# Optimization experiments

Hardware: AMD Instinct MI355X
Metric: run time of the kernel (lower is better)

Reference implementation:

```python
import jax, jax.numpy as jnp
import numpy as np

HEAD_SIZE = 64   # baseChn * max_channel_ratio
NUM_HEADS = 2
LEAKY_ALPHA = 0.3  # tf.keras.layers.LeakyReLU default


def setup_inputs() -> dict:
    key = jax.random.key(0)
    ks = jax.random.split(key, 6)
    x = jax.random.normal(ks[0], (96, 48, 512), dtype=jnp.float32)
    y = jax.random.uniform(ks[1], (96, 64, 64), dtype=jnp.float32)
    nItem = jax.random.uniform(ks[2], (96,), dtype=jnp.float32, minval=1.0, maxval=48.0)
    W_proj = jax.random.normal(ks[3], (512, 64), dtype=jnp.float32) * 0.05
    W1 = jax.random.normal(ks[4], (64, 128), dtype=jnp.float32) * 0.1
    W2 = jax.random.normal(ks[5], (2, 1), dtype=jnp.float32)
    return {"x": x, "y": y, "nItem": nItem, "W_proj": W_proj, "W1": W1, "W2": W2}


def reference(x, y, nItem, W_proj, W1, W2):
    # fc_cnn_proj: Dense(64, gelu exact, no bias)
    gallery = jax.nn.gelu(jnp.matmul(x, W_proj), approximate=False)  # [Sx, Nx, 64]
    Sx, Nx, _ = gallery.shape
    Sy, Ny, _ = y.shape
    sqrt_hs = jnp.sqrt(jnp.float32(HEAD_SIZE))
    # shared linear (no bias) then split heads: [S, H, N, hs]
    px = jnp.matmul(gallery, W1).reshape(Sx, Nx, NUM_HEADS, HEAD_SIZE).transpose(0, 2, 1, 3)
    py = jnp.matmul(y, W1).reshape(Sy, Ny, NUM_HEADS, HEAD_SIZE).transpose(0, 2, 1, 3)
    # pairwise cross-set attention maps: [Sy, Sx, H, Ny, Nx]
    att = jnp.einsum('yhmd,xhnd->yxhmn', py, px) / sqrt_hs
    att = jnp.where(att > 0, att, LEAKY_ALPHA * att)
    # reduce over both item axes, normalize by nItem[x] and nItemMax_y
    sc = att.sum(axis=(3, 4)) / nItem[None, :, None] / jnp.float32(Ny)  # [Sy, Sx, H]
    scores = jnp.matmul(sc, W2)  # linear2: Dense(1, no bias) -> [Sy, Sx, 1]
    return scores
```

## Files before the change

kernel.cpp:

```cpp
#include <hip/hip_runtime.h>
#include <hip/hip_bf16.h>


typedef short bf16x8 __attribute__((ext_vector_type(8)));
typedef float f32x4 __attribute__((ext_vector_type(4)));

__device__ __forceinline__ unsigned short f2bf(float v) {
  __hip_bfloat16 b = __float2bfloat16(v);
  return *reinterpret_cast<unsigned short*>(&b);
}

__device__ __forceinline__ bf16x8 load8_cvt(const float* __restrict__ p) {
  f32x4 v0 = *reinterpret_cast<const f32x4*>(p);
  f32x4 v1 = *reinterpret_cast<const f32x4*>(p + 4);
  bf16x8 r;
  r[0] = (short)f2bf(v0[0]); r[1] = (short)f2bf(v0[1]);
  r[2] = (short)f2bf(v0[2]); r[3] = (short)f2bf(v0[3]);
  r[4] = (short)f2bf(v1[0]); r[5] = (short)f2bf(v1[1]);
  r[6] = (short)f2bf(v1[2]); r[7] = (short)f2bf(v1[3]);
  return r;
}

__global__ __launch_bounds__(256) void k_wprep(const float* __restrict__ Wp,
                                               const float* __restrict__ W1,
                                               unsigned short* __restrict__ WpF,
                                               unsigned short* __restrict__ W1F) {
  int tid = blockIdx.x * 256 + threadIdx.x;
  if (tid < 32768) {
    int kc = tid >> 11, nt = (tid >> 9) & 3, l = (tid >> 3) & 63, i = tid & 7;
    int k = 32 * kc + 8 * (l >> 4) + i, c = nt * 16 + (l & 15);
    WpF[tid] = f2bf(Wp[k * 64 + c]);
  } else {
    int t2 = tid - 32768;
    int kc = t2 >> 12, nt = (t2 >> 9) & 7, l = (t2 >> 3) & 63, i = t2 & 7;
    int k = 32 * kc + 8 * (l >> 4) + i, d = nt * 16 + (l & 15);
    W1F[t2] = f2bf(W1[k * 128 + d]);
  }
}

__global__ __launch_bounds__(256, 3) void k_prep2(const float* __restrict__ x,
                                                  const float* __restrict__ y,
                                                  const unsigned short* __restrict__ WpF_u,
                                                  const unsigned short* __restrict__ W1F_u,
                                                  unsigned short* __restrict__ pyf,
                                                  unsigned short* __restrict__ pxf) {
  __shared__ unsigned short w1f[8192];
  __shared__ unsigned short wpq[16384];
  __shared__ unsigned short gal[32 * 72];
  int t = threadIdx.x;
  int lane = t & 63, w = t >> 6;
  int b = blockIdx.x;

  const bf16x8* W1Fg = reinterpret_cast<const bf16x8*>(W1F_u);
  const bf16x8* WPFg = reinterpret_cast<const bf16x8*>(WpF_u);
  const bf16x8* WF = reinterpret_cast<const bf16x8*>(w1f);
  const bf16x8* WPQ = reinterpret_cast<const bf16x8*>(wpq);

#pragma unroll
  for (int it = 0; it < 4; ++it)
    reinterpret_cast<bf16x8*>(w1f)[it * 256 + t] = W1Fg[it * 256 + t];

  f32x4 zero4 = {0.f, 0.f, 0.f, 0.f};
  asm volatile("" : "+v"(zero4));

  if (b < 144) {
    int rowbase = b * 32;
    int rt = w & 1, ntp = (w >> 1) * 2;
    const float* xa = x + (size_t)(rowbase + rt * 16 + (lane & 15)) * 512 + 8 * (lane >> 4);
    f32x4 acc[2] = {{0, 0, 0, 0}, {0, 0, 0, 0}};
#pragma unroll
    for (int hf = 0; hf < 2; ++hf) {
      if (hf) __syncthreads();
#pragma unroll
      for (int it = 0; it < 8; ++it)
        reinterpret_cast<bf16x8*>(wpq)[it * 256 + t] = WPFg[hf * 2048 + it * 256 + t];
      __syncthreads();
#pragma unroll
      for (int kcl = 0; kcl < 8; ++kcl) {
        bf16x8 a = load8_cvt(xa + 32 * (hf * 8 + kcl));
#pragma unroll
        for (int u = 0; u < 2; ++u)
          acc[u] = __builtin_amdgcn_mfma_f32_16x16x32_bf16(a, WPQ[(kcl * 4 + ntp + u) * 64 + lane], acc[u], 0, 0, 0);
      }
    }
#pragma unroll
    for (int u = 0; u < 2; ++u)
#pragma unroll
      for (int j = 0; j < 4; ++j) {
        float s = acc[u][j];
        float ge = 0.5f * s * (1.0f + erff(s * 0.70710678118654752f));
        int lr = rt * 16 + (lane >> 4) * 4 + j;
        int c = (ntp + u) * 16 + (lane & 15);
        gal[lr * 72 + c] = f2bf(ge);
      }
    __syncthreads();
    int nb = (w >> 1) * 4;
    const unsigned short* gp = &gal[(rt * 16 + (lane & 15)) * 72 + 8 * (lane >> 4)];
    bf16x8 g0 = *reinterpret_cast<const bf16x8*>(gp);
    bf16x8 g1 = *reinterpret_cast<const bf16x8*>(gp + 32);
#pragma unroll
    for (int v = 0; v < 4; ++v) {
      int nt2 = nb + v;
      f32x4 acc2 = __builtin_amdgcn_mfma_f32_16x16x32_bf16(g0, WF[nt2 * 64 + lane], zero4, 0, 0, 0);
      acc2 = __builtin_amdgcn_mfma_f32_16x16x32_bf16(g1, WF[(8 + nt2) * 64 + lane], acc2, 0, 0, 0);
      int d = nt2 * 16 + (lane & 15);
      int h = d >> 6, dd = d & 63;
      int kc = dd >> 5, q2 = (dd >> 3) & 3, i = dd & 7;
#pragma unroll
      for (int j = 0; j < 4; ++j) {
        int row = rowbase + rt * 16 + (lane >> 4) * 4 + j;
        int xi = row / 48, n = row % 48;
        int nt3 = n >> 4, rr = n & 15;
        size_t idx = ((size_t)((xi * 2 + h) * 6 + nt3 * 2 + kc)) * 512 + (rr + (q2 << 4)) * 8 + i;
        pxf[idx] = f2bf(acc2[j]);
      }
    }
  } else {
    __syncthreads();
    int b2 = b - 144;
    int mt = w & 1, nb = (w >> 1) * 4;
    const float* ybp = y + (size_t)(b2 * 32 + mt * 16 + (lane & 15)) * 64 + 8 * (lane >> 4);
    bf16x8 a0 = load8_cvt(ybp);
    bf16x8 a1 = load8_cvt(ybp + 32);
#pragma unroll
    for (int v = 0; v < 4; ++v) {
      int nt2 = nb + v;
      f32x4 acc = __builtin_amdgcn_mfma_f32_16x16x32_bf16(a0, WF[nt2 * 64 + lane], zero4, 0, 0, 0);
      acc = __builtin_amdgcn_mfma_f32_16x16x32_bf16(a1, WF[(8 + nt2) * 64 + lane], acc, 0, 0, 0);
      int d = nt2 * 16 + (lane & 15);
      int h = d >> 6, dd = d & 63;
      int kc = dd >> 5, q2 = (dd >> 3) & 3, i = dd & 7;
#pragma unroll
      for (int j = 0; j < 4; ++j) {
        int row = b2 * 32 + mt * 16 + (lane >> 4) * 4 + j;
        int yi = row >> 6, m = row & 63;
        int mt3 = m >> 4, rr = m & 15;
        size_t idx = ((size_t)((yi * 2 + h) * 8 + mt3 * 2 + kc)) * 512 + (rr + (q2 << 4)) * 8 + i;
        pyf[idx] = f2bf(acc[j]);
      }
    }
  }
}

__global__ __launch_bounds__(256) void k_att(const unsigned short* __restrict__ pyf_u,
                                             const unsigned short* __restrict__ pxf_u,
                                             const float* __restrict__ nItem,
                                             const float* __restrict__ W2,
                                             float* __restrict__ out) {
  int lane = threadIdx.x & 63;
  int w = threadIdx.x >> 6;
  int bid = blockIdx.x;
  int yb = bid >> 5, xq = bid & 31;
  int yi = yb * 4 + w;
  int xi0 = xq * 3;
  const bf16x8* PA = reinterpret_cast<const bf16x8*>(pyf_u);
  const bf16x8* PB = reinterpret_cast<const bf16x8*>(pxf_u);

  float w2h0 = W2[0], w2h1 = W2[1];
  float nI0 = nItem[xi0], nI1 = nItem[xi0 + 1], nI2 = nItem[xi0 + 2];

  f32x4 zero4 = {0.f, 0.f, 0.f, 0.f};
  asm volatile("" : "+v"(zero4));

  bf16x8 A8[16];
  size_t abase = (size_t)(yi * 2) * 512 + lane;
#pragma unroll
  for (int f = 0; f < 8; ++f) {
    A8[f]     = PA[abase + f * 64];
    A8[8 + f] = PA[abase + 512 + f * 64];
  }
  float c3h0 = 0.3f * w2h0, c7h0 = 0.7f * w2h0;
  float c3h1 = 0.3f * w2h1, c7h1 = 0.7f * w2h1;

  bf16x8 Bc[6], Bn[6];
  size_t bb0 = (size_t)((xi0 * 2 + 0) * 6) * 64 + lane;
#pragma unroll
  for (int f = 0; f < 6; ++f) Bc[f] = PB[bb0 + f * 64];

  f32x4 res4[3];
#pragma unroll
  for (int g = 0; g < 3; ++g) res4[g] = (f32x4){0.f, 0.f, 0.f, 0.f};

#pragma unroll
  for (int s = 0; s < 6; ++s) {
    const int h = s / 3, g = s % 3;
    if (s < 5) {
      const int s2 = s + 1, h2 = s2 / 3, g2 = s2 % 3;
      size_t bb = (size_t)(((xi0 + g2) * 2 + h2) * 6) * 64 + lane;
#pragma unroll
      for (int f = 0; f < 6; ++f) Bn[f] = PB[bb + f * 64];
    }
    const float c3 = h ? c3h1 : c3h0;
    const float c7 = h ? c7h1 : c7h0;
#pragma unroll
    for (int nt = 0; nt < 3; ++nt)
#pragma unroll
      for (int mt = 0; mt < 4; ++mt) {
        f32x4 acc = __builtin_amdgcn_mfma_f32_16x16x32_bf16(A8[h * 8 + mt * 2], Bc[nt * 2], zero4, 0, 0, 0);
        acc = __builtin_amdgcn_mfma_f32_16x16x32_bf16(A8[h * 8 + mt * 2 + 1], Bc[nt * 2 + 1], acc, 0, 0, 0);
        f32x4 mx = {fmaxf(acc[0], 0.f), fmaxf(acc[1], 0.f), fmaxf(acc[2], 0.f), fmaxf(acc[3], 0.f)};
        res4[g] += acc * c3;
        res4[g] += mx * c7;
      }
#pragma unroll
    for (int f = 0; f < 6; ++f) Bc[f] = Bn[f];
  }

  float tot0 = (res4[0][0] + res4[0][1]) + (res4[0][2] + res4[0][3]);
  float tot1 = (res4[1][0] + res4[1][1]) + (res4[1][2] + res4[1][3]);
  float tot2 = (res4[2][0] + res4[2][1]) + (res4[2][2] + res4[2][3]);
#pragma unroll
  for (int off = 32; off >= 1; off >>= 1) {
    tot0 += __shfl_xor(tot0, off, 64);
    tot1 += __shfl_xor(tot1, off, 64);
    tot2 += __shfl_xor(tot2, off, 64);
  }
  if (lane == 0) {
    out[yi * 96 + xi0 + 0] = tot0 / (512.0f * nI0);
    out[yi * 96 + xi0 + 1] = tot1 / (512.0f * nI1);
    out[yi * 96 + xi0 + 2] = tot2 / (512.0f * nI2);
  }
}

extern "C" void kernel_launch(void* const* d_in, const int* in_sizes, int n_in,
                              void* d_out, int out_size, void* d_ws, size_t ws_size,
                              hipStream_t stream) {
  const float* x     = (const float*)d_in[0];
  const float* y     = (const float*)d_in[1];
  const float* nItem = (const float*)d_in[2];
  const float* Wp    = (const float*)d_in[3];
  const float* W1    = (const float*)d_in[4];
  const float* W2    = (const float*)d_in[5];
  float* out = (float*)d_out;

  unsigned short* WpF = (unsigned short*)d_ws;
  unsigned short* W1F = WpF + 32768;
  unsigned short* pyf = W1F + 8192;
  unsigned short* pxf = pyf + 786432;

  hipLaunchKernelGGL(k_wprep, dim3(160), dim3(256), 0, stream, Wp, W1, WpF, W1F);
  hipLaunchKernelGGL(k_prep2, dim3(336), dim3(256), 0, stream, x, y, WpF, W1F, pyf, pxf);
  hipLaunchKernelGGL(k_att, dim3(768), dim3(256), 0, stream, pyf, pxf, nItem, W2, out);
}
```

Measured before the change: 38.64 us.

## Fuse weight bf16 conversion into prep kernel and drop separate weight-prep launch

Removes the standalone kernel that converted and reordered W_proj and W1 into bf16 MFMA fragment layout. Each prep block now reads the fp32 weights directly and converts and scatters them into shared memory itself, with W_proj staged in four quarter-sized chunks. This eliminates one kernel launch and its dependency barrier. In exchange, every one of the 336 blocks redoes the weight conversion, issuing scalar ushort scatter stores to LDS plus extra syncs.

```diff
diff --git a/kernel.cpp b/kernel.cpp
--- a/kernel.cpp
+++ b/kernel.cpp
@@ -21,44 +21,30 @@
   return r;
 }
 
-__global__ __launch_bounds__(256) void k_wprep(const float* __restrict__ Wp,
-                                               const float* __restrict__ W1,
-                                               unsigned short* __restrict__ WpF,
-                                               unsigned short* __restrict__ W1F) {
-  int tid = blockIdx.x * 256 + threadIdx.x;
-  if (tid < 32768) {
-    int kc = tid >> 11, nt = (tid >> 9) & 3, l = (tid >> 3) & 63, i = tid & 7;
-    int k = 32 * kc + 8 * (l >> 4) + i, c = nt * 16 + (l & 15);
-    WpF[tid] = f2bf(Wp[k * 64 + c]);
-  } else {
-    int t2 = tid - 32768;
-    int kc = t2 >> 12, nt = (t2 >> 9) & 7, l = (t2 >> 3) & 63, i = t2 & 7;
-    int k = 32 * kc + 8 * (l >> 4) + i, d = nt * 16 + (l & 15);
-    W1F[t2] = f2bf(W1[k * 128 + d]);
-  }
-}
-
-__global__ __launch_bounds__(256, 3) void k_prep2(const float* __restrict__ x,
+__global__ __launch_bounds__(256, 3) void k_prep3(const float* __restrict__ x,
                                                   const float* __restrict__ y,
-                                                  const unsigned short* __restrict__ WpF_u,
-                                                  const unsigned short* __restrict__ W1F_u,
+                                                  const float* __restrict__ Wp,
+                                                  const float* __restrict__ W1,
                                                   unsigned short* __restrict__ pyf,
                                                   unsigned short* __restrict__ pxf) {
   __shared__ unsigned short w1f[8192];
-  __shared__ unsigned short wpq[16384];
+  __shared__ unsigned short wpq[8192];
   __shared__ unsigned short gal[32 * 72];
   int t = threadIdx.x;
   int lane = t & 63, w = t >> 6;
   int b = blockIdx.x;
 
-  const bf16x8* W1Fg = reinterpret_cast<const bf16x8*>(W1F_u);
-  const bf16x8* WPFg = reinterpret_cast<const bf16x8*>(WpF_u);
   const bf16x8* WF = reinterpret_cast<const bf16x8*>(w1f);
   const bf16x8* WPQ = reinterpret_cast<const bf16x8*>(wpq);
 
 #pragma unroll
-  for (int it = 0; it < 4; ++it)
-    reinterpret_cast<bf16x8*>(w1f)[it * 256 + t] = W1Fg[it * 256 + t];
+  for (int it = 0; it < 32; ++it) {
+    int idx = it * 256 + t;
+    int k = idx >> 7, d = idx & 127;
+    int l = (d & 15) + 16 * ((k >> 3) & 3);
+    int f = (k >> 5) * 8 + (d >> 4);
+    w1f[f * 512 + l * 8 + (k & 7)] = f2bf(W1[idx]);
+  }
 
   f32x4 zero4 = {0.f, 0.f, 0.f, 0.f};
   asm volatile("" : "+v"(zero4));
@@ -69,18 +55,23 @@
     const float* xa = x + (size_t)(rowbase + rt * 16 + (lane & 15)) * 512 + 8 * (lane >> 4);
     f32x4 acc[2] = {{0, 0, 0, 0}, {0, 0, 0, 0}};
 #pragma unroll
-    for (int hf = 0; hf < 2; ++hf) {
-      if (hf) __syncthreads();
-#pragma unroll
-      for (int it = 0; it < 8; ++it)
-        reinterpret_cast<bf16x8*>(wpq)[it * 256 + t] = WPFg[hf * 2048 + it * 256 + t];
+    for (int q = 0; q < 4; ++q) {
+      if (q) __syncthreads();
+#pragma unroll
+      for (int it = 0; it < 32; ++it) {
+        int idx = it * 256 + t;
+        int kq = idx >> 6, c = idx & 63;
+        int l = (c & 15) + 16 * ((kq >> 3) & 3);
+        int g = ((kq >> 5) & 3) * 4 + (c >> 4);
+        wpq[g * 512 + l * 8 + (kq & 7)] = f2bf(Wp[(q * 128 + kq) * 64 + c]);
+      }
       __syncthreads();
 #pragma unroll
-      for (int kcl = 0; kcl < 8; ++kcl) {
-        bf16x8 a = load8_cvt(xa + 32 * (hf * 8 + kcl));
+      for (int kk = 0; kk < 4; ++kk) {
+        bf16x8 a = load8_cvt(xa + 32 * (q * 4 + kk));
 #pragma unroll
         for (int u = 0; u < 2; ++u)
-          acc[u] = __builtin_amdgcn_mfma_f32_16x16x32_bf16(a, WPQ[(kcl * 4 + ntp + u) * 64 + lane], acc[u], 0, 0, 0);
+          acc[u] = __builtin_amdgcn_mfma_f32_16x16x32_bf16(a, WPQ[(kk * 4 + ntp + u) * 64 + lane], acc[u], 0, 0, 0);
       }
     }
 #pragma unroll
@@ -233,12 +224,9 @@
   const float* W2    = (const float*)d_in[5];
   float* out = (float*)d_out;
 
-  unsigned short* WpF = (unsigned short*)d_ws;
-  unsigned short* W1F = WpF + 32768;
-  unsigned short* pyf = W1F + 8192;
+  unsigned short* pyf = (unsigned short*)d_ws;
   unsigned short* pxf = pyf + 786432;
 
-  hipLaunchKernelGGL(k_wprep, dim3(160), dim3(256), 0, stream, Wp, W1, WpF, W1F);
-  hipLaunchKernelGGL(k_prep2, dim3(336), dim3(256), 0, stream, x, y, WpF, W1F, pyf, pxf);
+  hipLaunchKernelGGL(k_prep3, dim3(336), dim3(256), 0, stream, x, y, Wp, W1, pyf, pxf);
   hipLaunchKernelGGL(k_att, dim3(768), dim3(256), 0, stream, pyf, pxf, nItem, W2, out);
 }
```

Result: slower. 48.47 us (+25.4%).

## Make projection kernel wave-independent, reading weights directly from global memory

Applied to the files above, without the earlier changes.

The projection kernel changes from block-cooperative tiles with weights staged in shared memory and block barriers to one 16-row tile per wavefront. Each wave computes all 64 gallery columns and all 128 projected columns itself, loading the weight fragments straight from global memory (L2/L1 cached), and uses a per-wave shared scratch for the GELU output with no __syncthreads. This removes the shared-memory weight staging and the block-level synchronisation, and shrinks LDS use so more blocks can be resident per CU. In exchange it issues more redundant global weight reads per wave, and each wave carries more accumulator registers and does more serial MFMA work.

```diff
diff --git a/kernel.cpp b/kernel.cpp
--- a/kernel.cpp
+++ b/kernel.cpp
@@ -38,77 +38,55 @@
   }
 }
 
-__global__ __launch_bounds__(256, 3) void k_prep2(const float* __restrict__ x,
-                                                  const float* __restrict__ y,
-                                                  const unsigned short* __restrict__ WpF_u,
-                                                  const unsigned short* __restrict__ W1F_u,
-                                                  unsigned short* __restrict__ pyf,
-                                                  unsigned short* __restrict__ pxf) {
-  __shared__ unsigned short w1f[8192];
-  __shared__ unsigned short wpq[16384];
-  __shared__ unsigned short gal[32 * 72];
-  int t = threadIdx.x;
-  int lane = t & 63, w = t >> 6;
-  int b = blockIdx.x;
-
-  const bf16x8* W1Fg = reinterpret_cast<const bf16x8*>(W1F_u);
-  const bf16x8* WPFg = reinterpret_cast<const bf16x8*>(WpF_u);
-  const bf16x8* WF = reinterpret_cast<const bf16x8*>(w1f);
-  const bf16x8* WPQ = reinterpret_cast<const bf16x8*>(wpq);
-
-#pragma unroll
-  for (int it = 0; it < 4; ++it)
-    reinterpret_cast<bf16x8*>(w1f)[it * 256 + t] = W1Fg[it * 256 + t];
+__global__ __launch_bounds__(256) void k_prep4(const float* __restrict__ x,
+                                               const float* __restrict__ y,
+                                               const unsigned short* __restrict__ WpF_u,
+                                               const unsigned short* __restrict__ W1F_u,
+                                               unsigned short* __restrict__ pyf,
+                                               unsigned short* __restrict__ pxf) {
+  __shared__ unsigned short gal[4][1152];
+  int lane = threadIdx.x & 63, w = threadIdx.x >> 6;
+  int wid = blockIdx.x * 4 + w;
+  const bf16x8* WPF = reinterpret_cast<const bf16x8*>(WpF_u);
+  const bf16x8* W1F = reinterpret_cast<const bf16x8*>(W1F_u);
 
   f32x4 zero4 = {0.f, 0.f, 0.f, 0.f};
   asm volatile("" : "+v"(zero4));
 
-  if (b < 144) {
-    int rowbase = b * 32;
-    int rt = w & 1, ntp = (w >> 1) * 2;
-    const float* xa = x + (size_t)(rowbase + rt * 16 + (lane & 15)) * 512 + 8 * (lane >> 4);
-    f32x4 acc[2] = {{0, 0, 0, 0}, {0, 0, 0, 0}};
-#pragma unroll
-    for (int hf = 0; hf < 2; ++hf) {
-      if (hf) __syncthreads();
-#pragma unroll
-      for (int it = 0; it < 8; ++it)
-        reinterpret_cast<bf16x8*>(wpq)[it * 256 + t] = WPFg[hf * 2048 + it * 256 + t];
-      __syncthreads();
-#pragma unroll
-      for (int kcl = 0; kcl < 8; ++kcl) {
-        bf16x8 a = load8_cvt(xa + 32 * (hf * 8 + kcl));
-#pragma unroll
-        for (int u = 0; u < 2; ++u)
-          acc[u] = __builtin_amdgcn_mfma_f32_16x16x32_bf16(a, WPQ[(kcl * 4 + ntp + u) * 64 + lane], acc[u], 0, 0, 0);
-      }
-    }
-#pragma unroll
-    for (int u = 0; u < 2; ++u)
+  if (wid < 288) {
+    int rowbase = wid * 16;
+    const float* xa = x + (size_t)(rowbase + (lane & 15)) * 512 + 8 * (lane >> 4);
+    f32x4 acc[4];
+#pragma unroll
+    for (int nt = 0; nt < 4; ++nt) acc[nt] = (f32x4){0.f, 0.f, 0.f, 0.f};
+#pragma unroll
+    for (int kc = 0; kc < 16; ++kc) {
+      bf16x8 a = load8_cvt(xa + 32 * kc);
+#pragma unroll
+      for (int nt = 0; nt < 4; ++nt)
+        acc[nt] = __builtin_amdgcn_mfma_f32_16x16x32_bf16(a, WPF[(kc * 4 + nt) * 64 + lane], acc[nt], 0, 0, 0);
+    }
+#pragma unroll
+    for (int nt = 0; nt < 4; ++nt)
 #pragma unroll
       for (int j = 0; j < 4; ++j) {
-        float s = acc[u][j];
+        float s = acc[nt][j];
         float ge = 0.5f * s * (1.0f + erff(s * 0.70710678118654752f));
-        int lr = rt * 16 + (lane >> 4) * 4 + j;
-        int c = (ntp + u) * 16 + (lane & 15);
-        gal[lr * 72 + c] = f2bf(ge);
-      }
-    __syncthreads();
-    int nb = (w >> 1) * 4;
-    const unsigned short* gp = &gal[(rt * 16 + (lane & 15)) * 72 + 8 * (lane >> 4)];
+        gal[w][((lane >> 4) * 4 + j) * 72 + nt * 16 + (lane & 15)] = f2bf(ge);
+      }
+    const unsigned short* gp = &gal[w][(lane & 15) * 72 + 8 * (lane >> 4)];
     bf16x8 g0 = *reinterpret_cast<const bf16x8*>(gp);
     bf16x8 g1 = *reinterpret_cast<const bf16x8*>(gp + 32);
 #pragma unroll
-    for (int v = 0; v < 4; ++v) {
-      int nt2 = nb + v;
-      f32x4 acc2 = __builtin_amdgcn_mfma_f32_16x16x32_bf16(g0, WF[nt2 * 64 + lane], zero4, 0, 0, 0);
-      acc2 = __builtin_amdgcn_mfma_f32_16x16x32_bf16(g1, WF[(8 + nt2) * 64 + lane], acc2, 0, 0, 0);
+    for (int nt2 = 0; nt2 < 8; ++nt2) {
+      f32x4 acc2 = __builtin_amdgcn_mfma_f32_16x16x32_bf16(g0, W1F[nt2 * 64 + lane], zero4, 0, 0, 0);
+      acc2 = __builtin_amdgcn_mfma_f32_16x16x32_bf16(g1, W1F[(8 + nt2) * 64 + lane], acc2, 0, 0, 0);
       int d = nt2 * 16 + (lane & 15);
       int h = d >> 6, dd = d & 63;
       int kc = dd >> 5, q2 = (dd >> 3) & 3, i = dd & 7;
 #pragma unroll
       for (int j = 0; j < 4; ++j) {
-        int row = rowbase + rt * 16 + (lane >> 4) * 4 + j;
+        int row = rowbase + (lane >> 4) * 4 + j;
         int xi = row / 48, n = row % 48;
         int nt3 = n >> 4, rr = n & 15;
         size_t idx = ((size_t)((xi * 2 + h) * 6 + nt3 * 2 + kc)) * 512 + (rr + (q2 << 4)) * 8 + i;
@@ -116,23 +94,20 @@
       }
     }
   } else {
-    __syncthreads();
-    int b2 = b - 144;
-    int mt = w & 1, nb = (w >> 1) * 4;
-    const float* ybp = y + (size_t)(b2 * 32 + mt * 16 + (lane & 15)) * 64 + 8 * (lane >> 4);
+    int row0 = (wid - 288) * 16;
+    const float* ybp = y + (size_t)(row0 + (lane & 15)) * 64 + 8 * (lane >> 4);
     bf16x8 a0 = load8_cvt(ybp);
     bf16x8 a1 = load8_cvt(ybp + 32);
 #pragma unroll
-    for (int v = 0; v < 4; ++v) {
-      int nt2 = nb + v;
-      f32x4 acc = __builtin_amdgcn_mfma_f32_16x16x32_bf16(a0, WF[nt2 * 64 + lane], zero4, 0, 0, 0);
-      acc = __builtin_amdgcn_mfma_f32_16x16x32_bf16(a1, WF[(8 + nt2) * 64 + lane], acc, 0, 0, 0);
+    for (int nt2 = 0; nt2 < 8; ++nt2) {
+      f32x4 acc = __builtin_amdgcn_mfma_f32_16x16x32_bf16(a0, W1F[nt2 * 64 + lane], zero4, 0, 0, 0);
+      acc = __builtin_amdgcn_mfma_f32_16x16x32_bf16(a1, W1F[(8 + nt2) * 64 + lane], acc, 0, 0, 0);
       int d = nt2 * 16 + (lane & 15);
       int h = d >> 6, dd = d & 63;
       int kc = dd >> 5, q2 = (dd >> 3) & 3, i = dd & 7;
 #pragma unroll
       for (int j = 0; j < 4; ++j) {
-        int row = b2 * 32 + mt * 16 + (lane >> 4) * 4 + j;
+        int row = row0 + (lane >> 4) * 4 + j;
         int yi = row >> 6, m = row & 63;
         int mt3 = m >> 4, rr = m & 15;
         size_t idx = ((size_t)((yi * 2 + h) * 8 + mt3 * 2 + kc)) * 512 + (rr + (q2 << 4)) * 8 + i;
@@ -239,6 +214,6 @@
   unsigned short* pxf = pyf + 786432;
 
   hipLaunchKernelGGL(k_wprep, dim3(160), dim3(256), 0, stream, Wp, W1, WpF, W1F);
-  hipLaunchKernelGGL(k_prep2, dim3(336), dim3(256), 0, stream, x, y, WpF, W1F, pyf, pxf);
+  hipLaunchKernelGGL(k_prep4, dim3(168), dim3(256), 0, stream, x, y, WpF, W1F, pyf, pxf);
   hipLaunchKernelGGL(k_att, dim3(768), dim3(256), 0, stream, pyf, pxf, nItem, W2, out);
 }
```

Result: faster. 37.43 us (-3.1%).
